# Kernel optimization log

Measured on AMD Instinct MI355X. Metric: run time of the kernel, lower is better.

Reference implementation:

```python
import jax, jax.numpy as jnp
import numpy as np

TAU = 0.1

def setup_inputs() -> dict:
    key = jax.random.key(0)
    kZ, k1, k2 = jax.random.split(key, 3)
    N, D = 8192, 128
    scale = 1.0 / np.sqrt(D)
    return {
        "Z": jax.random.normal(kZ, (N, D), dtype=jnp.float32),
        "W1": jax.random.normal(k1, (D, D), dtype=jnp.float32) * scale,
        "b1": jnp.zeros((D,), dtype=jnp.float32),
        "W2": jax.random.normal(k2, (D, D), dtype=jnp.float32) * scale,
        "b2": jnp.zeros((D,), dtype=jnp.float32),
    }

def reference(Z, W1, b1, W2, b2):
    # DiffusivityTransform: 2-layer MLP with ReLU (torch Linear: x @ W.T + b;
    # here W1/W2 are stored already transposed as [in, out])
    t = jax.nn.relu(Z @ W1 + b1) @ W2 + b2          # [N, D]
    sim = t @ t.T                                     # [N, N]
    S = jax.nn.softmax(sim, axis=1)                   # row-stochastic [N, N]
    Z_prop = S @ Z                                    # [N, D]
    return Z + TAU * (Z_prop - Z)
```

## Files before the change

### kernel.cpp

```cpp
#include <hip/hip_runtime.h>

typedef _Float16 half_t;
typedef _Float16 hx8 __attribute__((ext_vector_type(8)));
typedef _Float16 hx4 __attribute__((ext_vector_type(4)));
typedef float fx4 __attribute__((ext_vector_type(4)));

#define LOG2E 1.44269504088896f
#define TAU 0.1f
#define NSPLIT 16

__global__ __launch_bounds__(256) void prep_kernel(
    const float* __restrict__ W1, const float* __restrict__ W2,
    const float* __restrict__ Z,
    half_t* __restrict__ W1t, half_t* __restrict__ W2t,
    half_t* __restrict__ Zth)
{
  __shared__ float tile[32*132];
  const int bx = blockIdx.x;
  const int tid = threadIdx.x;
  if (bx < 8) {
    const float* W = (bx & 4) ? W2 : W1;
    half_t* Wt = (bx & 4) ? W2t : W1t;
    const int i0 = (bx & 3) * 32;
    const int r = tid >> 3, cb = tid & 7;
#pragma unroll
    for (int it=0; it<4; ++it) {
      int c4 = cb*4 + it*32;
      *(fx4*)(&tile[r*132 + c4]) = *(const fx4*)(W + (size_t)(i0+r)*128 + c4);
    }
    __syncthreads();
    const int o = tid >> 1, ih = (tid & 1)*16;
    hx8 v0, v1;
#pragma unroll
    for (int u=0;u<8;++u) v0[u] = (half_t)tile[(ih+u)*132 + o];
#pragma unroll
    for (int u=0;u<8;++u) v1[u] = (half_t)tile[(ih+8+u)*132 + o];
    *(hx8*)(Wt + (size_t)o*128 + i0 + ih)     = v0;
    *(hx8*)(Wt + (size_t)o*128 + i0 + ih + 8) = v1;
  } else {
    float* zt = tile;
    const int b = bx - 8;
    const int nb = b >> 2;
    const int db = b & 3;
#pragma unroll
    for (int i=0;i<2;++i) {
      int fid = i*256 + tid;
      int r = fid >> 3, c4 = (fid & 7) * 4;
      *(fx4*)(&zt[r*36 + c4]) = *(const fx4*)(Z + (size_t)(nb*64 + r)*128 + db*32 + c4);
    }
    __syncthreads();
    const int cr = tid >> 3, j = tid & 7, n0 = j*8;
    hx8 hv;
#pragma unroll
    for (int idx=0;idx<8;++idx) hv[idx] = (half_t)zt[(n0+idx)*36 + cr];
    *(hx8*)(Zth + (size_t)(db*32 + cr)*8192 + nb*64 + n0) = hv;
  }
}

__global__ __launch_bounds__(128) void mlp_kernel(
    const float* __restrict__ Z, const half_t* __restrict__ W1t,
    const float* __restrict__ b1, const half_t* __restrict__ W2t,
    const float* __restrict__ b2, half_t* __restrict__ T)
{
  __shared__ half_t Hs[2][16*136];
  const int tid = threadIdx.x;
  const int w = tid >> 6, lane = tid & 63;
  const int q = lane >> 4, c = lane & 15;
  const int wrow = blockIdx.x*32 + w*16;

  hx8 zb[4];
#pragma unroll
  for (int ks=0;ks<4;++ks) {
    fx4 a = *(const fx4*)(Z + (size_t)(wrow + c)*128 + ks*32 + q*8);
    fx4 b = *(const fx4*)(Z + (size_t)(wrow + c)*128 + ks*32 + q*8 + 4);
#pragma unroll
    for (int u=0;u<4;++u) { zb[ks][u] = (half_t)a[u]; zb[ks][4+u] = (half_t)b[u]; }
  }
  fx4 acc[8];
#pragma unroll
  for (int mt=0;mt<8;++mt) acc[mt] = (fx4){0.f,0.f,0.f,0.f};
#pragma unroll
  for (int mt=0;mt<8;++mt)
#pragma unroll
    for (int ks=0;ks<4;++ks) {
      hx8 aw = *(const hx8*)(W1t + (size_t)(mt*16 + c)*128 + ks*32 + q*8);
      acc[mt] = __builtin_amdgcn_mfma_f32_16x16x32_f16(aw, zb[ks], acc[mt], 0,0,0);
    }
#pragma unroll
  for (int mt=0;mt<8;++mt) {
    fx4 bias = *(const fx4*)(b1 + mt*16 + 4*q);
    hx4 hv;
#pragma unroll
    for (int i=0;i<4;++i) {
      float h = acc[mt][i] + bias[i];
      hv[i] = (half_t)(h > 0.f ? h : 0.f);
    }
    *(hx4*)(&Hs[w][c*136 + mt*16 + 4*q]) = hv;
  }

  hx8 hb[4];
#pragma unroll
  for (int ks=0;ks<4;++ks) hb[ks] = *(const hx8*)(&Hs[w][c*136 + ks*32 + q*8]);
#pragma unroll
  for (int mt=0;mt<8;++mt) acc[mt] = (fx4){0.f,0.f,0.f,0.f};
#pragma unroll
  for (int mt=0;mt<8;++mt)
#pragma unroll
    for (int ks=0;ks<4;++ks) {
      hx8 aw = *(const hx8*)(W2t + (size_t)(mt*16 + c)*128 + ks*32 + q*8);
      acc[mt] = __builtin_amdgcn_mfma_f32_16x16x32_f16(aw, hb[ks], acc[mt], 0,0,0);
    }
#pragma unroll
  for (int mt=0;mt<8;++mt) {
    fx4 bias = *(const fx4*)(b2 + mt*16 + 4*q);
    hx4 tv;
#pragma unroll
    for (int i=0;i<4;++i) tv[i] = (half_t)(acc[mt][i] + bias[i]);
    *(hx4*)(T + (size_t)(wrow + c)*128 + mt*16 + 4*q) = tv;
  }
}

__global__ __launch_bounds__(256,2) void flash_kernel(
    const half_t* __restrict__ T, const half_t* __restrict__ Zt,
    half_t* __restrict__ Pacc, float* __restrict__ Pm, float* __restrict__ Pl)
{
  __shared__ half_t Tks[16*512];
  __shared__ half_t Zts[16*512];
  const int tid = threadIdx.x;
  const int w = tid >> 6, lane = tid & 63;
  const int q = lane >> 4, c = lane & 15;
  const int bx = blockIdx.x;
  const int qb = bx >> 4, kh = bx & 15;
  const int wrow = qb*128 + w*32;
  half_t* Psw = &Tks[w*2048];
  const int sw = (c & 7) * 8;

  hx8 bq[2][4];
#pragma unroll
  for (int nt=0;nt<2;++nt)
#pragma unroll
    for (int ks=0;ks<4;++ks)
      bq[nt][ks] = *(const hx8*)(T + (size_t)(wrow + nt*16 + c)*128 + ks*32 + q*8);

  fx4 oacc[8][2];
#pragma unroll
  for (int mtd=0;mtd<8;++mtd)
#pragma unroll
    for (int nt=0;nt<2;++nt) oacc[mtd][nt] = (fx4){0.f,0.f,0.f,0.f};
  float m_run[2] = {-1e30f,-1e30f};
  float l_run[2] = {0.f,0.f};

  hx8 pre[8];
  const int kbase = kh*512;

  auto load_tile = [&](int kt0) {
    if (w < 2) {
#pragma unroll
      for (int i=0;i<8;++i) {
        int f = w*8 + i, mt = f >> 2, ks = f & 3;
        pre[i] = *(const hx8*)(T + (size_t)(kt0 + mt*16 + c)*128 + ks*32 + q*8);
      }
    } else {
#pragma unroll
      for (int i=0;i<8;++i) {
        int f2 = (w-2)*8 + i, mtd = f2 >> 1, ks2 = f2 & 1;
        pre[i] = *(const hx8*)(Zt + (size_t)(mtd*16 + c)*8192 + kt0 + ks2*32 + q*8);
      }
    }
  };
  auto store_tile = [&]() {
    if (w < 2) {
#pragma unroll
      for (int i=0;i<8;++i) { int f = w*8 + i; *(hx8*)(&Tks[f*512 + lane*8]) = pre[i]; }
    } else {
#pragma unroll
      for (int i=0;i<8;++i) { int f2 = (w-2)*8 + i; *(hx8*)(&Zts[f2*512 + lane*8]) = pre[i]; }
    }
  };

  load_tile(kbase);
  for (int t=0;t<8;++t) {
    __syncthreads();
    store_tile();
    __syncthreads();
    if (t < 7) load_tile(kbase + (t+1)*64);

    fx4 sacc[4][2];
#pragma unroll
    for (int mt=0;mt<4;++mt)
#pragma unroll
      for (int nt=0;nt<2;++nt) sacc[mt][nt] = (fx4){0.f,0.f,0.f,0.f};
#pragma unroll
    for (int ks=0;ks<4;++ks)
#pragma unroll
      for (int mt=0;mt<4;++mt) {
        hx8 ak = *(const hx8*)(&Tks[(mt*4+ks)*512 + lane*8]);
        sacc[mt][0] = __builtin_amdgcn_mfma_f32_16x16x32_f16(ak, bq[0][ks], sacc[mt][0], 0,0,0);
        sacc[mt][1] = __builtin_amdgcn_mfma_f32_16x16x32_f16(ak, bq[1][ks], sacc[mt][1], 0,0,0);
      }

    hx4 pk[2][4];
#pragma unroll
    for (int nt=0;nt<2;++nt) {
      float mx = -1e30f;
#pragma unroll
      for (int mt=0;mt<4;++mt)
#pragma unroll
        for (int i=0;i<4;++i) mx = fmaxf(mx, sacc[mt][nt][i]);
      mx = fmaxf(mx, __shfl_xor(mx, 16, 64));
      mx = fmaxf(mx, __shfl_xor(mx, 32, 64));
      float mnew = fmaxf(m_run[nt], mx);
      float alpha = __builtin_amdgcn_exp2f((m_run[nt]-mnew)*LOG2E);
      m_run[nt] = mnew;
      float nb = mnew*LOG2E;
      float rs = 0.f;
#pragma unroll
      for (int mt=0;mt<4;++mt) {
#pragma unroll
        for (int i=0;i<4;++i) {
          float p = __builtin_amdgcn_exp2f(sacc[mt][nt][i]*LOG2E - nb);
          rs += p;
          pk[nt][mt][i] = (half_t)p;
        }
      }
      rs += __shfl_xor(rs, 16, 64);
      rs += __shfl_xor(rs, 32, 64);
      l_run[nt] = l_run[nt]*alpha + rs;
#pragma unroll
      for (int mtd=0;mtd<8;++mtd)
#pragma unroll
        for (int i=0;i<4;++i) oacc[mtd][nt][i] *= alpha;
    }

    __syncthreads();
#pragma unroll
    for (int nt=0;nt<2;++nt)
#pragma unroll
      for (int mt=0;mt<4;++mt)
        *(hx4*)(&Psw[(nt*16 + c)*64 + ((mt*16 + 4*q) ^ sw)]) = pk[nt][mt];

#pragma unroll
    for (int ks2=0;ks2<2;++ks2) {
      hx8 bp0 = *(const hx8*)(&Psw[(c     )*64 + ((ks2*32 + q*8) ^ sw)]);
      hx8 bp1 = *(const hx8*)(&Psw[(16 + c)*64 + ((ks2*32 + q*8) ^ sw)]);
#pragma unroll
      for (int mtd=0;mtd<8;++mtd) {
        hx8 az = *(const hx8*)(&Zts[(mtd*2+ks2)*512 + lane*8]);
        oacc[mtd][0] = __builtin_amdgcn_mfma_f32_16x16x32_f16(az, bp0, oacc[mtd][0], 0,0,0);
        oacc[mtd][1] = __builtin_amdgcn_mfma_f32_16x16x32_f16(az, bp1, oacc[mtd][1], 0,0,0);
      }
    }
  }

#pragma unroll
  for (int nt=0;nt<2;++nt) {
    float inv = 1.0f / l_run[nt];
    const size_t rowg = (size_t)(bx*128 + w*32 + nt*16 + c);
#pragma unroll
    for (int mtd=0;mtd<8;++mtd) {
      hx4 ov;
#pragma unroll
      for (int i=0;i<4;++i) ov[i] = (half_t)(oacc[mtd][nt][i]*inv);
      *(hx4*)(Pacc + rowg*128 + mtd*16 + 4*q) = ov;
    }
    if (q == 0) {
      Pm[rowg] = m_run[nt];
      Pl[rowg] = l_run[nt];
    }
  }
}

__global__ __launch_bounds__(256) void merge_kernel(
    const float* __restrict__ Z, const half_t* __restrict__ Pacc,
    const float* __restrict__ Pm, const float* __restrict__ Pl,
    float* __restrict__ out)
{
  const int th = blockIdx.x*256 + threadIdx.x;
  const int r = th >> 5, cg = th & 31;
  const int qb = r >> 7, rr = r & 127;
  float mk[NSPLIT], lk[NSPLIT];
  float M = -1e30f;
#pragma unroll
  for (int k=0;k<NSPLIT;++k) {
    int p = qb*NSPLIT + k;
    mk[k] = Pm[p*128 + rr];
    lk[k] = Pl[p*128 + rr];
    M = fmaxf(M, mk[k]);
  }
  float L = 0.f, wk[NSPLIT];
#pragma unroll
  for (int k=0;k<NSPLIT;++k) { wk[k] = lk[k]*__builtin_amdgcn_exp2f((mk[k]-M)*LOG2E); L += wk[k]; }
  float o0=0.f,o1=0.f,o2=0.f,o3=0.f;
#pragma unroll
  for (int k=0;k<NSPLIT;++k) {
    int p = qb*NSPLIT + k;
    hx4 v = *(const hx4*)(Pacc + ((size_t)p*128 + rr)*128 + cg*4);
    o0 += wk[k]*(float)v[0]; o1 += wk[k]*(float)v[1];
    o2 += wk[k]*(float)v[2]; o3 += wk[k]*(float)v[3];
  }
  float invL = 1.0f / L;
  fx4 zv = *(const fx4*)(Z + (size_t)r*128 + cg*4);
  fx4 res;
  res[0] = (1.f-TAU)*zv[0] + TAU*o0*invL;
  res[1] = (1.f-TAU)*zv[1] + TAU*o1*invL;
  res[2] = (1.f-TAU)*zv[2] + TAU*o2*invL;
  res[3] = (1.f-TAU)*zv[3] + TAU*o3*invL;
  *(fx4*)(out + (size_t)r*128 + cg*4) = res;
}

extern "C" void kernel_launch(void* const* d_in, const int* in_sizes, int n_in,
                              void* d_out, int out_size, void* d_ws, size_t ws_size,
                              hipStream_t stream) {
  const float* Z  = (const float*)d_in[0];
  const float* W1 = (const float*)d_in[1];
  const float* b1 = (const float*)d_in[2];
  const float* W2 = (const float*)d_in[3];
  const float* b2 = (const float*)d_in[4];
  float* out = (float*)d_out;

  char* ws = (char*)d_ws;
  const size_t NBLK = 64 * NSPLIT;
  half_t* Thi  = (half_t*)(ws);
  half_t* Zth  = (half_t*)(ws + (size_t)2*1024*1024);
  half_t* Pacc = (half_t*)(ws + (size_t)4*1024*1024);
  float*  Pm   = (float*)(ws + (size_t)4*1024*1024 + NBLK*128*128*2);
  float*  Pl   = Pm + NBLK*128;
  half_t* W1t  = (half_t*)(ws + (size_t)4*1024*1024 + NBLK*128*128*2 + 2*NBLK*128*4);
  half_t* W2t  = W1t + 128*128;

  hipLaunchKernelGGL(prep_kernel,  dim3(520),  dim3(256), 0, stream, W1, W2, Z, W1t, W2t, Zth);
  hipLaunchKernelGGL(mlp_kernel,   dim3(256),  dim3(128), 0, stream, Z, W1t, b1, W2t, b2, Thi);
  hipLaunchKernelGGL(flash_kernel, dim3(NBLK), dim3(256), 0, stream, Thi, Zth, Pacc, Pm, Pl);
  hipLaunchKernelGGL(merge_kernel, dim3(1024), dim3(256), 0, stream, Z, Pacc, Pm, Pl, out);
}
```

Measured before the change: 143.3 us.

## Double-buffer flash tiles with async global-to-LDS loads and halve key splits

Replaces the register-staged tile load and LDS store with direct global-to-LDS async loads (global_load_lds) into a ping-pong pair of T and Z buffers. The next tile is issued right after the softmax barrier, so it overlaps the P·Z MFMA phase, and one barrier per iteration goes away. The key-dimension split drops from 16 to 8, so each block walks 16 tiles instead of 8 and there are fewer partial results to merge. In exchange LDS per block doubles to 64KB and grid parallelism halves. Correctness also relies on the barrier waiting for the async LDS writes to finish.

```diff
diff --git a/kernel.cpp b/kernel.cpp
--- a/kernel.cpp
+++ b/kernel.cpp
@@ -7,7 +7,7 @@
 
 #define LOG2E 1.44269504088896f
 #define TAU 0.1f
-#define NSPLIT 16
+#define NSPLIT 8
 
 __global__ __launch_bounds__(256) void prep_kernel(
     const float* __restrict__ W1, const float* __restrict__ W2,
@@ -124,15 +124,14 @@
     const half_t* __restrict__ T, const half_t* __restrict__ Zt,
     half_t* __restrict__ Pacc, float* __restrict__ Pm, float* __restrict__ Pl)
 {
-  __shared__ half_t Tks[16*512];
-  __shared__ half_t Zts[16*512];
+  __shared__ half_t Tbuf[2][16*512];
+  __shared__ half_t Zbuf[2][16*512];
   const int tid = threadIdx.x;
   const int w = tid >> 6, lane = tid & 63;
   const int q = lane >> 4, c = lane & 15;
   const int bx = blockIdx.x;
-  const int qb = bx >> 4, kh = bx & 15;
+  const int qb = bx >> 3, kh = bx & 7;
   const int wrow = qb*128 + w*32;
-  half_t* Psw = &Tks[w*2048];
   const int sw = (c & 7) * 8;
 
   hx8 bq[2][4];
@@ -150,40 +149,40 @@
   float m_run[2] = {-1e30f,-1e30f};
   float l_run[2] = {0.f,0.f};
 
-  hx8 pre[8];
-  const int kbase = kh*512;
-
-  auto load_tile = [&](int kt0) {
+  const int kbase = kh*1024;
+
+  auto issue_loads = [&](int kt0, int b) {
     if (w < 2) {
 #pragma unroll
       for (int i=0;i<8;++i) {
         int f = w*8 + i, mt = f >> 2, ks = f & 3;
-        pre[i] = *(const hx8*)(T + (size_t)(kt0 + mt*16 + c)*128 + ks*32 + q*8);
+        const half_t* gp = T + (size_t)(kt0 + mt*16 + c)*128 + ks*32 + q*8;
+        half_t* lp = &Tbuf[b][f*512 + lane*8];
+        __builtin_amdgcn_global_load_lds(
+            (const __attribute__((address_space(1))) void*)gp,
+            (__attribute__((address_space(3))) void*)lp, 16, 0, 0);
       }
     } else {
 #pragma unroll
       for (int i=0;i<8;++i) {
         int f2 = (w-2)*8 + i, mtd = f2 >> 1, ks2 = f2 & 1;
-        pre[i] = *(const hx8*)(Zt + (size_t)(mtd*16 + c)*8192 + kt0 + ks2*32 + q*8);
+        const half_t* gp = Zt + (size_t)(mtd*16 + c)*8192 + kt0 + ks2*32 + q*8;
+        half_t* lp = &Zbuf[b][f2*512 + lane*8];
+        __builtin_amdgcn_global_load_lds(
+            (const __attribute__((address_space(1))) void*)gp,
+            (__attribute__((address_space(3))) void*)lp, 16, 0, 0);
       }
     }
   };
-  auto store_tile = [&]() {
-    if (w < 2) {
-#pragma unroll
-      for (int i=0;i<8;++i) { int f = w*8 + i; *(hx8*)(&Tks[f*512 + lane*8]) = pre[i]; }
-    } else {
-#pragma unroll
-      for (int i=0;i<8;++i) { int f2 = (w-2)*8 + i; *(hx8*)(&Zts[f2*512 + lane*8]) = pre[i]; }
-    }
-  };
-
-  load_tile(kbase);
-  for (int t=0;t<8;++t) {
+
+  issue_loads(kbase, 0);
+
+  for (int t=0;t<16;++t) {
+    const int cur = t & 1;
     __syncthreads();
-    store_tile();
-    __syncthreads();
-    if (t < 7) load_tile(kbase + (t+1)*64);
+    half_t* Tcur = Tbuf[cur];
+    half_t* Zcur = Zbuf[cur];
+    half_t* Psw  = &Tbuf[cur][w*2048];
 
     fx4 sacc[4][2];
 #pragma unroll
@@ -194,7 +193,7 @@
     for (int ks=0;ks<4;++ks)
 #pragma unroll
       for (int mt=0;mt<4;++mt) {
-        hx8 ak = *(const hx8*)(&Tks[(mt*4+ks)*512 + lane*8]);
+        hx8 ak = *(const hx8*)(&Tcur[(mt*4+ks)*512 + lane*8]);
         sacc[mt][0] = __builtin_amdgcn_mfma_f32_16x16x32_f16(ak, bq[0][ks], sacc[mt][0], 0,0,0);
         sacc[mt][1] = __builtin_amdgcn_mfma_f32_16x16x32_f16(ak, bq[1][ks], sacc[mt][1], 0,0,0);
       }
@@ -233,6 +232,8 @@
     }
 
     __syncthreads();
+    if (t < 15) issue_loads(kbase + (t+1)*64, cur ^ 1);
+
 #pragma unroll
     for (int nt=0;nt<2;++nt)
 #pragma unroll
@@ -245,7 +246,7 @@
       hx8 bp1 = *(const hx8*)(&Psw[(16 + c)*64 + ((ks2*32 + q*8) ^ sw)]);
 #pragma unroll
       for (int mtd=0;mtd<8;++mtd) {
-        hx8 az = *(const hx8*)(&Zts[(mtd*2+ks2)*512 + lane*8]);
+        hx8 az = *(const hx8*)(&Zcur[(mtd*2+ks2)*512 + lane*8]);
         oacc[mtd][0] = __builtin_amdgcn_mfma_f32_16x16x32_f16(az, bp0, oacc[mtd][0], 0,0,0);
         oacc[mtd][1] = __builtin_amdgcn_mfma_f32_16x16x32_f16(az, bp1, oacc[mtd][1], 0,0,0);
       }
```

Measured after the change: 131.6 us. 8.2% less time.
